# Kernel optimization log

Measured on AMD Instinct MI355X. Metric: run time of the kernel, lower is better.

Reference implementation:

```python
import jax, jax.numpy as jnp
import numpy as np

# dims: P planes, N planar nodes/plane, M nexus nodes, E edges/plane, C classes
P, N, M, E, C, FP, FN = 3, 100000, 30000, 200000, 5, 64, 32


def class_linear(x, W, b):
    # x: [..., C, in], W: [C, out, in], b: [C, out] -> [..., C, out]
    return jnp.einsum('...ci,coi->...co', x, W) + b


def setup_inputs() -> dict:
    key = jax.random.key(0)
    ks = jax.random.split(key, 12)
    def nrm(k, shape, scale=1.0):
        return jax.random.normal(k, shape, jnp.float32) * scale
    return {
        'x': nrm(ks[0], (P, N, C, FP)),
        'nexus': nrm(ks[1], (M, C, FN)),
        'edge_src': jax.random.randint(ks[2], (P, E), 0, N, jnp.int32),
        'edge_dst': jax.random.randint(ks[3], (P, E), 0, M, jnp.int32),
        'Wn1': nrm(ks[4], (C, FN, P * FP), (P * FP) ** -0.5),
        'bn1': jnp.zeros((C, FN), jnp.float32),
        'Wn2': nrm(ks[5], (C, FN, FN), FN ** -0.5),
        'bn2': jnp.zeros((C, FN), jnp.float32),
        'We': nrm(ks[6], (P, C, 1, FP + FN), (FP + FN) ** -0.5),
        'be': jnp.zeros((P, C, 1), jnp.float32),
        'Wd1': nrm(ks[7], (P, C, FP, FP + FN), (FP + FN) ** -0.5),
        'bd1': jnp.zeros((P, C, FP), jnp.float32),
        'Wd2': nrm(ks[8], (P, C, FP, FP), FP ** -0.5),
        'bd2': jnp.zeros((P, C, FP), jnp.float32),
    }


def reference(x, nexus, edge_src, edge_dst, Wn1, bn1, Wn2, bn2,
              We, be, Wd1, bd1, Wd2, bd2):
    # --- nexus_up: SimpleConv (sum-aggregate planar features at nexus nodes) ---
    def up_one(xp, src, dst):
        return jax.ops.segment_sum(xp[src], dst, num_segments=M)  # [M,C,FP]
    up = jax.vmap(up_one)(x, edge_src, edge_dst)                   # [P,M,C,FP]
    # torch.cat(n, dim=-1) over planes -> [M, C, P*FP]
    n_cat = jnp.transpose(up, (1, 2, 0, 3)).reshape(M, C, P * FP)

    # --- nexus_net: ClassLinear -> tanh -> ClassLinear -> tanh ---
    n = jnp.tanh(class_linear(n_cat, Wn1, bn1))
    n = jnp.tanh(class_linear(n, Wn2, bn2))                        # [M,C,FN]

    # --- nexus_down per plane (flow target_to_source, aggr mean at src) ---
    def down_one(xp, src, dst, We_p, be_p, W1, b1, W2, b2):
        x_i = xp[src]                                              # [E,C,FP]
        n_j = n[dst]                                               # [E,C,FN]
        feat = jax.lax.stop_gradient(jnp.concatenate([x_i, n_j], -1))
        # per-class scalar logit, softmax over class dim (dim=1)
        w = jax.nn.softmax(class_linear(feat, We_p, be_p), axis=1)  # [E,C,1]
        msg = w * n_j                                               # [E,C,FN]
        s = jax.ops.segment_sum(msg, src, num_segments=N)           # [N,C,FN]
        cnt = jax.ops.segment_sum(jnp.ones((E,), msg.dtype), src, num_segments=N)
        aggr = s / jnp.maximum(cnt, 1.0)[:, None, None]             # scatter-mean
        h = jnp.tanh(class_linear(jnp.concatenate([xp, aggr], -1), W1, b1))
        return jnp.tanh(class_linear(h, W2, b2))                    # [N,C,FP]

    out = jax.vmap(down_one)(x, edge_src, edge_dst, We, be, Wd1, bd1, Wd2, bd2)
    return out  # [P,N,C,FP] updated planar embeddings (x['u'],x['v'],x['y'])
```

## Files before the change

kernel.cpp:

```cpp
#include <hip/hip_runtime.h>
#include <hip/hip_fp16.h>

#define P_ 3
#define N_ 100000
#define M_ 30000
#define E_ 200000
#define C_ 5
#define FP_ 64
#define FN_ 32
#define PFP_ 192
#define FPFN_ 96
#define PE_ 600000
#define PN_ 300000
#define PM_ 90000
#define NT_ 64
#define TILES_ ((N_ + NT_ - 1) / NT_)
#define NTD_ 128
#define TILESD_ ((N_ + NTD_ - 1) / NTD_)
#define CFN_ 160
#define NW1_ 92160
#define NW2_ 61440
#define NWN1_ 30720
#define NB_S_ ((PN_ + 1023) / 1024)
#define NB_D_ ((PM_ + 1023) / 1024)
#define NB_CNT_ ((PE_ + 255) / 256)
#define NB_WC_ ((NW1_ + 255) / 256)
#define NB_PROJ_ (P_ * TILES_)
#define NB_FILL_ ((PE_ + 511) / 512)

typedef _Float16 f16x8 __attribute__((ext_vector_type(8)));
typedef float f32x4 __attribute__((ext_vector_type(4)));

__device__ __forceinline__ float fast_tanh(float v) {
  float t = __expf(2.0f * v);
  return 1.0f - __fdividef(2.0f, t + 1.0f);
}

__device__ __forceinline__ f16x8 ld8(const __half* p) {
  return *(const f16x8*)(const void*)p;
}

__global__ void k_countw(const int* __restrict__ esrc, const int* __restrict__ edst,
                         int* __restrict__ cnt_src, int* __restrict__ cnt_dst,
                         const float* __restrict__ Wd1, const float* __restrict__ Wd2,
                         const float* __restrict__ Wn1,
                         __half* __restrict__ w1h, __half* __restrict__ w2h,
                         __half* __restrict__ wn1h) {
  int b = blockIdx.x;
  if (b < NB_CNT_) {
    int i = b * 256 + threadIdx.x;
    if (i >= PE_) return;
    int p = i / E_;
    atomicAdd(&cnt_src[p * N_ + esrc[i]], 1);
    atomicAdd(&cnt_dst[p * M_ + edst[i]], 1);
  } else {
    int i = (b - NB_CNT_) * 256 + threadIdx.x;
    if (i < NW1_) w1h[i] = __float2half(Wd1[i]);
    if (i < NW2_) w2h[i] = __float2half(Wd2[i]);
    if (i < NWN1_) wn1h[i] = __float2half(Wn1[i]);
  }
}

__global__ void k_scan1c(const int* __restrict__ in_s, int* __restrict__ out_s,
                         int* __restrict__ aux_s,
                         const int* __restrict__ in_d, int* __restrict__ out_d,
                         int* __restrict__ aux_d) {
  __shared__ int lds[256];
  int b = blockIdx.x, t = threadIdx.x;
  const int* in;
  int* out;
  int* aux;
  int n;
  if (b < NB_S_) { in = in_s; out = out_s; aux = aux_s; n = PN_; }
  else           { b -= NB_S_; in = in_d; out = out_d; aux = aux_d; n = PM_; }
  int base = b * 1024 + t * 4;
  int v0 = (base + 0 < n) ? in[base + 0] : 0;
  int v1 = (base + 1 < n) ? in[base + 1] : 0;
  int v2 = (base + 2 < n) ? in[base + 2] : 0;
  int v3 = (base + 3 < n) ? in[base + 3] : 0;
  lds[t] = v0 + v1 + v2 + v3;
  __syncthreads();
  for (int off = 1; off < 256; off <<= 1) {
    int xv = (t >= off) ? lds[t - off] : 0;
    __syncthreads();
    lds[t] += xv;
    __syncthreads();
  }
  if (t == 255) aux[b] = lds[255];
  int run = (t == 0) ? 0 : lds[t - 1];
  if (base + 0 < n) out[base + 0] = run; run += v0;
  if (base + 1 < n) out[base + 1] = run; run += v1;
  if (base + 2 < n) out[base + 2] = run; run += v2;
  if (base + 3 < n) out[base + 3] = run;
}

__global__ void k_scan2c(int* __restrict__ aux_s, int* __restrict__ end_s,
                         int* __restrict__ aux_d, int* __restrict__ end_d) {
  __shared__ int lds[1024];
  int t = threadIdx.x;
  int* aux = (blockIdx.x == 0) ? aux_s : aux_d;
  int* offe = (blockIdx.x == 0) ? end_s : end_d;
  int nb = (blockIdx.x == 0) ? NB_S_ : NB_D_;
  lds[t] = (t < nb) ? aux[t] : 0;
  __syncthreads();
  for (int off = 1; off < 1024; off <<= 1) {
    int xv = (t >= off) ? lds[t - off] : 0;
    __syncthreads();
    lds[t] += xv;
    __syncthreads();
  }
  if (t < nb) aux[t] = (t == 0) ? 0 : lds[t - 1];
  if (t == 0) offe[0] = lds[nb - 1];
}

__global__ void k_scan3c(int* __restrict__ off_s, const int* __restrict__ aux_s,
                         int* __restrict__ cur_s,
                         int* __restrict__ off_d, const int* __restrict__ aux_d,
                         int* __restrict__ cur_d) {
  int i = blockIdx.x * 256 + threadIdx.x;
  if (i < PN_) {
    int v = off_s[i] + aux_s[i >> 10];
    off_s[i] = v;
    cur_s[i] = v;
  } else if (i < PN_ + PM_) {
    int j = i - PN_;
    int v = off_d[j] + aux_d[j >> 10];
    off_d[j] = v;
    cur_d[j] = v;
  }
}

__global__ __launch_bounds__(512) void k_projfill(
    const float* __restrict__ x, const __half* __restrict__ wn1h,
    const float* __restrict__ We,
    __half* __restrict__ y, float* __restrict__ xdot,
    __half* __restrict__ xh, int write_xh,
    const int* __restrict__ esrc, const int* __restrict__ edst,
    int* __restrict__ cur_src, int* __restrict__ cur_dst,
    int* __restrict__ list_src, int* __restrict__ list_src_e,
    int* __restrict__ list_dst, int* __restrict__ list_dst_e) {
  __shared__ __align__(16) __half xs[NT_ * 320];
  int bp = blockIdx.x;
  int t = threadIdx.x;

  if (bp >= NB_PROJ_) {
    int i = (bp - NB_PROJ_) * 512 + t;
    if (i < PE_) {
      int p = i / E_;
      int s = esrc[i], d = edst[i];
      int ps = atomicAdd(&cur_src[p * N_ + s], 1);
      list_src[ps] = d;
      list_src_e[ps] = i;
      int pd = atomicAdd(&cur_dst[p * M_ + d], 1);
      list_dst[pd] = s;
      list_dst_e[pd] = i;
    }
    return;
  }

  int p = bp / TILES_, tile = bp % TILES_;
  int base = tile * NT_;
  int rows = min(NT_, N_ - base);

  const float* xb = x + (size_t)(p * N_ + base) * 320;
  __half* xo = xh + (size_t)(p * N_ + base) * 320;
  for (int idx = t; idx < rows * 40; idx += 512) {
    int row = idx / 40, col = idx % 40;
    const float4* s4 = (const float4*)&xb[row * 320 + col * 8];
    float4 v0 = s4[0], v1 = s4[1];
    union { __half2 h[4]; float4 f; } u4;
    u4.h[0] = __floats2half2_rn(v0.x, v0.y);
    u4.h[1] = __floats2half2_rn(v0.z, v0.w);
    u4.h[2] = __floats2half2_rn(v1.x, v1.y);
    u4.h[3] = __floats2half2_rn(v1.z, v1.w);
    *(float4*)&xs[row * 320 + ((col * 8) ^ ((row & 7) << 3))] = u4.f;
    if (write_xh) *(float4*)&xo[row * 320 + col * 8] = u4.f;
  }
  __syncthreads();

  int w = t >> 6, l = t & 63;
  int l15 = l & 15, l4 = l >> 4;
  int q4 = w & 3, ct = w >> 2;
  int nA = q4 * 16 + l15;
  int swzA = (nA & 7) << 3;

  #pragma unroll
  for (int c = 0; c < C_; ++c) {
    f16x8 a0 = ld8(&xs[nA * 320 + ((c * 64 + 0  + l4 * 8) ^ swzA)]);
    f16x8 a1 = ld8(&xs[nA * 320 + ((c * 64 + 32 + l4 * 8) ^ swzA)]);
    const __half* wb = &wn1h[(size_t)(c * 32 + ct * 16 + l15) * PFP_ + p * 64];
    f16x8 b0 = ld8(&wb[0  + l4 * 8]);
    f16x8 b1 = ld8(&wb[32 + l4 * 8]);
    f32x4 acc = (f32x4){0.f, 0.f, 0.f, 0.f};
    acc = __builtin_amdgcn_mfma_f32_16x16x32_f16(a0, b0, acc, 0, 0, 0);
    acc = __builtin_amdgcn_mfma_f32_16x16x32_f16(a1, b1, acc, 0, 0, 0);
    #pragma unroll
    for (int r = 0; r < 4; ++r) {
      int node = q4 * 16 + l4 * 4 + r;
      if (node < rows)
        y[(size_t)(p * N_ + base + node) * CFN_ + c * 32 + ct * 16 + l15] =
            __float2half(acc[r]);
    }
  }

  for (int idx = t; idx < C_ * NT_; idx += 512) {
    int cx = idx >> 6, nodex = idx & 63;
    if (nodex < rows) {
      int swz = (nodex & 7) << 3;
      const float2* wer = (const float2*)&We[(p * C_ + cx) * FPFN_];
      float s = 0.f;
      #pragma unroll
      for (int i = 0; i < 32; ++i) {
        __half2 xv = *(const __half2*)&xs[nodex * 320 + ((cx * 64 + 2 * i) ^ swz)];
        float2 wv = wer[i];
        s += __low2float(xv) * wv.x + __high2float(xv) * wv.y;
      }
      xdot[(size_t)(p * N_ + base + nodex) * C_ + cx] = s;
    }
  }
}

__global__ __launch_bounds__(320) void k_nexus(
    const __half* __restrict__ y,
    const int* __restrict__ off_dst, const int* __restrict__ list_dst,
    const int* __restrict__ list_dst_e, const int* __restrict__ esrc,
    const float* __restrict__ bn1,
    const float* __restrict__ Wn2, const float* __restrict__ bn2,
    const float* __restrict__ We,
    const float* __restrict__ xdot, const float* __restrict__ be,
    __half* __restrict__ nout, __half* __restrict__ wbuf) {
  __shared__ float part[16][CFN_];
  __shared__ __align__(16) float h1S[CFN_];
  __shared__ __align__(16) float h2S[CFN_];
  __shared__ float ndS[P_ * C_];
  __shared__ float beS[P_ * C_];
  int m = blockIdx.x;
  int t = threadIdx.x;
  int g = t / 20, u4 = t % 20;

  float acc[8];
  #pragma unroll
  for (int i = 0; i < 8; ++i) acc[i] = 0.f;
  #pragma unroll
  for (int p = 0; p < P_; ++p) {
    int o0 = off_dst[p * M_ + m];
    int o1 = off_dst[p * M_ + m + 1];
    const __half* yp = y + (size_t)p * N_ * CFN_;
    for (int e = o0 + g; e < o1; e += 16) {
      int s0 = list_dst[e];
      float4 v = *(const float4*)&yp[(size_t)s0 * CFN_ + u4 * 8];
      union { float4 f; __half2 h[4]; } uu;
      uu.f = v;
      #pragma unroll
      for (int i = 0; i < 4; ++i) {
        acc[2 * i]     += __low2float(uu.h[i]);
        acc[2 * i + 1] += __high2float(uu.h[i]);
      }
    }
  }
  #pragma unroll
  for (int i = 0; i < 8; ++i) part[g][u4 * 8 + i] = acc[i];
  __syncthreads();
  if (t < CFN_) {
    float pre = bn1[t];
    #pragma unroll
    for (int gg = 0; gg < 16; ++gg) pre += part[gg][t];
    h1S[t] = fast_tanh(pre);
  }
  __syncthreads();
  if (t < CFN_) {
    int c = t >> 5;
    const float4* f4 = (const float4*)&h1S[c * FN_];
    const float4* w4 = (const float4*)&Wn2[(size_t)t * FN_];
    float a = bn2[t];
    #pragma unroll
    for (int i = 0; i < FN_ / 4; ++i) {
      float4 f = f4[i], wv = w4[i];
      a += f.x * wv.x + f.y * wv.y + f.z * wv.z + f.w * wv.w;
    }
    float nv = fast_tanh(a);
    h2S[t] = nv;
    nout[(size_t)m * CFN_ + t] = __float2half(nv);
  }
  __syncthreads();
  if (t < P_ * C_) {
    int p = t / C_, cc = t % C_;
    const float* wv = &We[(p * C_ + cc) * FPFN_ + FP_];
    float a = 0.f;
    #pragma unroll
    for (int j = 0; j < FN_; ++j) a += h2S[cc * FN_ + j] * wv[j];
    ndS[t] = a;
    beS[t] = be[t];
  }
  __syncthreads();
  #pragma unroll
  for (int p = 0; p < P_; ++p) {
    int o0 = off_dst[p * M_ + m];
    int o1 = off_dst[p * M_ + m + 1];
    for (int e = o0 + t; e < o1; e += 320) {
      int i = list_dst_e[e];
      int src = esrc[i];
      const float* xd = &xdot[(size_t)(p * N_ + src) * C_];
      float lg[C_];
      #pragma unroll
      for (int cc = 0; cc < C_; ++cc) lg[cc] = xd[cc] + ndS[p * C_ + cc] + beS[p * C_ + cc];
      float mx = fmaxf(fmaxf(fmaxf(lg[0], lg[1]), fmaxf(lg[2], lg[3])), lg[4]);
      float s = 0.f;
      #pragma unroll
      for (int cc = 0; cc < C_; ++cc) { lg[cc] = __expf(lg[cc] - mx); s += lg[cc]; }
      float inv = __fdividef(1.0f, s);
      __half* wp = &wbuf[(size_t)i * C_];
      #pragma unroll
      for (int cc = 0; cc < C_; ++cc) wp[cc] = __float2half(lg[cc] * inv);
    }
  }
}

template<int XH>
__global__ __launch_bounds__(256, 6) void k_dec(
    const float* __restrict__ x, const __half* __restrict__ xh,
    const __half* __restrict__ nout, const __half* __restrict__ wbuf,
    const int* __restrict__ off_src, const int* __restrict__ list_src,
    const int* __restrict__ list_src_e,
    const __half* __restrict__ w1h, const float* __restrict__ bd1,
    const __half* __restrict__ w2h, const float* __restrict__ bd2,
    float* __restrict__ out) {
  __shared__ __align__(16) __half featS[NTD_ * 104];

  int bp = blockIdx.x;
  int pc = bp / TILESD_;
  int tile = bp % TILESD_;
  int p = pc / C_, c = pc % C_;
  int base = tile * NTD_;
  int rows = min(NTD_, N_ - base);

  int t = threadIdx.x;
  int w = t >> 6, l = t & 63;
  int l15 = l & 15, l4 = l >> 4;

  if constexpr (XH) {
    for (int idx = t; idx < NTD_ * 8; idx += 256) {
      int node = idx >> 3, q = idx & 7;
      if (node < rows) {
        float4 v = *(const float4*)&xh[(size_t)(p * N_ + base + node) * 320 + c * 64 + q * 8];
        *(float4*)&featS[node * 104 + q * 8] = v;
      }
    }
  } else {
    for (int idx = t; idx < NTD_ * 16; idx += 256) {
      int node = idx >> 4, fq = idx & 15;
      if (node < rows) {
        float4 v = *(const float4*)&x[(size_t)(p * N_ + base + node) * 320 + c * 64 + fq * 4];
        __half2* dst = (__half2*)&featS[node * 104 + fq * 4];
        dst[0] = __floats2half2_rn(v.x, v.y);
        dst[1] = __floats2half2_rn(v.z, v.w);
      }
    }
  }
  {
    int nd = t >> 1, hf = t & 1;
    if (nd < rows) {
      int pn = p * N_ + base + nd;
      int o0 = off_src[pn], o1 = off_src[pn + 1];
      __half2 acc[8];
      #pragma unroll
      for (int i = 0; i < 8; ++i) acc[i] = __floats2half2_rn(0.f, 0.f);
      for (int e = o0; e < o1; e += 2) {
        int e1 = e + 1;
        bool has1 = (e1 < o1);
        int d0 = list_src[e];
        int i0 = list_src_e[e];
        int d1 = list_src[has1 ? e1 : e];
        int i1 = list_src_e[has1 ? e1 : e];
        __half wg0h = wbuf[(size_t)i0 * C_ + c];
        __half wg1h = wbuf[(size_t)i1 * C_ + c];
        const __half2* nr0 = (const __half2*)&nout[(size_t)d0 * CFN_ + c * FN_ + hf * 16];
        const __half2* nr1 = (const __half2*)&nout[(size_t)d1 * CFN_ + c * FN_ + hf * 16];
        __half2 v0[8], v1[8];
        #pragma unroll
        for (int i = 0; i < 8; ++i) v0[i] = nr0[i];
        #pragma unroll
        for (int i = 0; i < 8; ++i) v1[i] = nr1[i];
        __half2 wg0 = __half2half2(wg0h);
        #pragma unroll
        for (int i = 0; i < 8; ++i) acc[i] = __hfma2(wg0, v0[i], acc[i]);
        if (has1) {
          __half2 wg1 = __half2half2(wg1h);
          #pragma unroll
          for (int i = 0; i < 8; ++i) acc[i] = __hfma2(wg1, v1[i], acc[i]);
        }
      }
      float invd = __fdividef(1.0f, fmaxf((float)(o1 - o0), 1.0f));
      __half2 invd2 = __float2half2_rn(invd);
      __half2* dst2 = (__half2*)&featS[nd * 104 + 64 + hf * 16];
      #pragma unroll
      for (int i = 0; i < 8; ++i) dst2[i] = __hmul2(acc[i], invd2);
    }
  }
  __syncthreads();

  int rbase = w * 32;
  const __half* w1g = w1h + (size_t)(p * C_ + c) * 64 * 96;
  const __half* w2g = w2h + (size_t)(p * C_ + c) * 64 * 64;

  f32x4 acc[2][4];
  #pragma unroll
  for (int tt = 0; tt < 4; ++tt) {
    float bv = bd1[(p * C_ + c) * FP_ + tt * 16 + l15];
    #pragma unroll
    for (int rt = 0; rt < 2; ++rt) acc[rt][tt] = (f32x4){bv, bv, bv, bv};
  }
  #pragma unroll
  for (int s = 0; s < 3; ++s) {
    f16x8 a0 = ld8(&featS[(rbase + l15) * 104 + s * 32 + l4 * 8]);
    f16x8 a1 = ld8(&featS[(rbase + 16 + l15) * 104 + s * 32 + l4 * 8]);
    #pragma unroll
    for (int tt = 0; tt < 4; ++tt) {
      f16x8 b = ld8(&w1g[(tt * 16 + l15) * 96 + s * 32 + l4 * 8]);
      acc[0][tt] = __builtin_amdgcn_mfma_f32_16x16x32_f16(a0, b, acc[0][tt], 0, 0, 0);
      acc[1][tt] = __builtin_amdgcn_mfma_f32_16x16x32_f16(a1, b, acc[1][tt], 0, 0, 0);
    }
  }
  #pragma unroll
  for (int rt = 0; rt < 2; ++rt)
    #pragma unroll
    for (int tt = 0; tt < 4; ++tt) {
      #pragma unroll
      for (int r = 0; r < 4; ++r) {
        int nrow = rbase + rt * 16 + l4 * 4 + r;
        featS[nrow * 104 + tt * 16 + l15] = __float2half(fast_tanh(acc[rt][tt][r]));
      }
    }

  f32x4 acc2[2][4];
  #pragma unroll
  for (int tt = 0; tt < 4; ++tt) {
    float bv = bd2[(p * C_ + c) * FP_ + tt * 16 + l15];
    #pragma unroll
    for (int rt = 0; rt < 2; ++rt) acc2[rt][tt] = (f32x4){bv, bv, bv, bv};
  }
  #pragma unroll
  for (int s = 0; s < 2; ++s) {
    f16x8 a0 = ld8(&featS[(rbase + l15) * 104 + s * 32 + l4 * 8]);
    f16x8 a1 = ld8(&featS[(rbase + 16 + l15) * 104 + s * 32 + l4 * 8]);
    #pragma unroll
    for (int tt = 0; tt < 4; ++tt) {
      f16x8 b = ld8(&w2g[(tt * 16 + l15) * 64 + s * 32 + l4 * 8]);
      acc2[0][tt] = __builtin_amdgcn_mfma_f32_16x16x32_f16(a0, b, acc2[0][tt], 0, 0, 0);
      acc2[1][tt] = __builtin_amdgcn_mfma_f32_16x16x32_f16(a1, b, acc2[1][tt], 0, 0, 0);
    }
  }
  #pragma unroll
  for (int rt = 0; rt < 2; ++rt)
    #pragma unroll
    for (int tt = 0; tt < 4; ++tt) {
      #pragma unroll
      for (int r = 0; r < 4; ++r) {
        int nrow = rbase + rt * 16 + l4 * 4 + r;
        int node = base + nrow;
        if (node < N_) {
          out[(size_t)(p * N_ + node) * 320 + c * 64 + tt * 16 + l15] =
              fast_tanh(acc2[rt][tt][r]);
        }
      }
    }
}

#define WS_Y      0ll
#define WS_NOUT   24000000ll
#define WS_LISTSE 26400000ll
#define WS_WBUF   27000000ll
#define WS_XDOT   28800000ll
#define WS_OFFS   30750000ll
#define WS_OFFD   31050001ll
#define WS_CURS   31140002ll
#define WS_CURD   31440002ll
#define WS_LISTS  31530002ll
#define WS_LISTD  32130002ll
#define WS_AUX1   32730002ll
#define WS_AUX2   32730514ll
#define WS_W1H    32731026ll
#define WS_W2H    32777106ll
#define WS_LISTDE 32808000ll
#define WS_WN1H   33408000ll
#define WS_XH     33423360ll
#define WS_XH_END_BYTES ((WS_XH + 48000000ll) * 4ll)

extern "C" void kernel_launch(void* const* d_in, const int* in_sizes, int n_in,
                              void* d_out, int out_size, void* d_ws, size_t ws_size,
                              hipStream_t stream) {
  const float* x   = (const float*)d_in[0];
  const int* esrc  = (const int*)d_in[2];
  const int* edst  = (const int*)d_in[3];
  const float* Wn1 = (const float*)d_in[4];
  const float* bn1 = (const float*)d_in[5];
  const float* Wn2 = (const float*)d_in[6];
  const float* bn2 = (const float*)d_in[7];
  const float* We  = (const float*)d_in[8];
  const float* be  = (const float*)d_in[9];
  const float* Wd1 = (const float*)d_in[10];
  const float* bd1 = (const float*)d_in[11];
  const float* Wd2 = (const float*)d_in[12];
  const float* bd2 = (const float*)d_in[13];
  float* out = (float*)d_out;

  float* wsf = (float*)d_ws;
  int*   wsi = (int*)d_ws;
  __half* ybuf = (__half*)d_ws;
  __half* nout = (__half*)(wsi + WS_NOUT);
  __half* wbuf = (__half*)(wsi + WS_WBUF);
  float* xdot = wsf + WS_XDOT;
  int* off_src = wsi + WS_OFFS;
  int* off_dst = wsi + WS_OFFD;
  int* cur_src = wsi + WS_CURS;
  int* cur_dst = wsi + WS_CURD;
  int* list_src = wsi + WS_LISTS;
  int* list_src_e = wsi + WS_LISTSE;
  int* list_dst = wsi + WS_LISTD;
  int* list_dst_e = wsi + WS_LISTDE;
  int* aux1 = wsi + WS_AUX1;
  int* aux2 = wsi + WS_AUX2;
  __half* w1h = (__half*)(wsi + WS_W1H);
  __half* w2h = (__half*)(wsi + WS_W2H);
  __half* wn1h = (__half*)(wsi + WS_WN1H);
  __half* xh  = (__half*)(wsi + WS_XH);

  int use_xh = (ws_size >= (size_t)WS_XH_END_BYTES) ? 1 : 0;

  hipMemsetAsync(cur_src, 0, (PN_ + PM_) * sizeof(int), stream);
  k_countw<<<NB_CNT_ + NB_WC_, 256, 0, stream>>>(esrc, edst, cur_src, cur_dst,
                                                 Wd1, Wd2, Wn1, w1h, w2h, wn1h);
  k_scan1c<<<NB_S_ + NB_D_, 256, 0, stream>>>(cur_src, off_src, aux1,
                                              cur_dst, off_dst, aux2);
  k_scan2c<<<2, 1024, 0, stream>>>(aux1, off_src + PN_, aux2, off_dst + PM_);
  k_scan3c<<<(PN_ + PM_ + 255) / 256, 256, 0, stream>>>(off_src, aux1, cur_src,
                                                        off_dst, aux2, cur_dst);

  k_projfill<<<NB_PROJ_ + NB_FILL_, 512, 0, stream>>>(
      x, wn1h, We, ybuf, xdot, xh, use_xh,
      esrc, edst, cur_src, cur_dst,
      list_src, list_src_e, list_dst, list_dst_e);

  k_nexus<<<M_, 320, 0, stream>>>(ybuf, off_dst, list_dst, list_dst_e, esrc,
                                  bn1, Wn2, bn2, We, xdot, be, nout, wbuf);

  if (use_xh) {
    k_dec<1><<<P_ * C_ * TILESD_, 256, 0, stream>>>(x, xh, nout, wbuf,
                                                    off_src, list_src, list_src_e,
                                                    w1h, bd1, w2h, bd2, out);
  } else {
    k_dec<0><<<P_ * C_ * TILESD_, 256, 0, stream>>>(x, xh, nout, wbuf,
                                                    off_src, list_src, list_src_e,
                                                    w1h, bd1, w2h, bd2, out);
  }
}
```

Before: 718.5 us.

## Store softmax weights in src-CSR order and prefetch first edges in decoder

The fill step now records each edge's position in the source-sorted CSR list instead of storing the edge id there. The nexus kernel writes softmax weights at that CSR position, so the decoder reads weights contiguously by CSR index and no longer needs the list_src_e indirection. The decoder also loads offsets, the first two neighbor ids and their weights before staging the x tile, so those latencies overlap the tile load. This trades a scattered read of pos_src in k_nexus for fewer dependent gathers in the decoder.

```diff
diff --git a/kernel.cpp b/kernel.cpp
--- a/kernel.cpp
+++ b/kernel.cpp
@@ -137,7 +137,7 @@
     __half* __restrict__ xh, int write_xh,
     const int* __restrict__ esrc, const int* __restrict__ edst,
     int* __restrict__ cur_src, int* __restrict__ cur_dst,
-    int* __restrict__ list_src, int* __restrict__ list_src_e,
+    int* __restrict__ list_src, int* __restrict__ pos_src,
     int* __restrict__ list_dst, int* __restrict__ list_dst_e) {
   __shared__ __align__(16) __half xs[NT_ * 320];
   int bp = blockIdx.x;
@@ -150,7 +150,7 @@
       int s = esrc[i], d = edst[i];
       int ps = atomicAdd(&cur_src[p * N_ + s], 1);
       list_src[ps] = d;
-      list_src_e[ps] = i;
+      pos_src[i] = ps;
       int pd = atomicAdd(&cur_dst[p * M_ + d], 1);
       list_dst[pd] = s;
       list_dst_e[pd] = i;
@@ -224,6 +224,7 @@
     const __half* __restrict__ y,
     const int* __restrict__ off_dst, const int* __restrict__ list_dst,
     const int* __restrict__ list_dst_e, const int* __restrict__ esrc,
+    const int* __restrict__ pos_src,
     const float* __restrict__ bn1,
     const float* __restrict__ Wn2, const float* __restrict__ bn2,
     const float* __restrict__ We,
@@ -300,6 +301,7 @@
     for (int e = o0 + t; e < o1; e += 320) {
       int i = list_dst_e[e];
       int src = esrc[i];
+      int pos = pos_src[i];
       const float* xd = &xdot[(size_t)(p * N_ + src) * C_];
       float lg[C_];
       #pragma unroll
@@ -309,7 +311,7 @@
       #pragma unroll
       for (int cc = 0; cc < C_; ++cc) { lg[cc] = __expf(lg[cc] - mx); s += lg[cc]; }
       float inv = __fdividef(1.0f, s);
-      __half* wp = &wbuf[(size_t)i * C_];
+      __half* wp = &wbuf[(size_t)pos * C_];
       #pragma unroll
       for (int cc = 0; cc < C_; ++cc) wp[cc] = __float2half(lg[cc] * inv);
     }
@@ -321,7 +323,6 @@
     const float* __restrict__ x, const __half* __restrict__ xh,
     const __half* __restrict__ nout, const __half* __restrict__ wbuf,
     const int* __restrict__ off_src, const int* __restrict__ list_src,
-    const int* __restrict__ list_src_e,
     const __half* __restrict__ w1h, const float* __restrict__ bd1,
     const __half* __restrict__ w2h, const float* __restrict__ bd2,
     float* __restrict__ out) {
@@ -337,6 +338,22 @@
   int t = threadIdx.x;
   int w = t >> 6, l = t & 63;
   int l15 = l & 15, l4 = l >> 4;
+
+  int nd = t >> 1, hf = t & 1;
+  int o0 = 0, o1 = 0, d0 = 0, d1 = 0;
+  __half wg0h = __float2half(0.f), wg1h = __float2half(0.f);
+  bool nact = (nd < rows);
+  if (nact) {
+    int pn = p * N_ + base + nd;
+    o0 = off_src[pn];
+    o1 = off_src[pn + 1];
+    int e1 = o0 + 1;
+    bool has1 = (e1 < o1);
+    d0 = (o0 < o1) ? list_src[o0] : 0;
+    d1 = has1 ? list_src[e1] : d0;
+    if (o0 < o1) wg0h = wbuf[(size_t)o0 * C_ + c];
+    if (has1)    wg1h = wbuf[(size_t)e1 * C_ + c];
+  }
 
   if constexpr (XH) {
     for (int idx = t; idx < NTD_ * 8; idx += 256) {
@@ -357,45 +374,41 @@
       }
     }
   }
-  {
-    int nd = t >> 1, hf = t & 1;
-    if (nd < rows) {
-      int pn = p * N_ + base + nd;
-      int o0 = off_src[pn], o1 = off_src[pn + 1];
-      __half2 acc[8];
-      #pragma unroll
-      for (int i = 0; i < 8; ++i) acc[i] = __floats2half2_rn(0.f, 0.f);
-      for (int e = o0; e < o1; e += 2) {
-        int e1 = e + 1;
-        bool has1 = (e1 < o1);
-        int d0 = list_src[e];
-        int i0 = list_src_e[e];
-        int d1 = list_src[has1 ? e1 : e];
-        int i1 = list_src_e[has1 ? e1 : e];
-        __half wg0h = wbuf[(size_t)i0 * C_ + c];
-        __half wg1h = wbuf[(size_t)i1 * C_ + c];
-        const __half2* nr0 = (const __half2*)&nout[(size_t)d0 * CFN_ + c * FN_ + hf * 16];
-        const __half2* nr1 = (const __half2*)&nout[(size_t)d1 * CFN_ + c * FN_ + hf * 16];
-        __half2 v0[8], v1[8];
+
+  if (nact) {
+    __half2 acc[8];
+    #pragma unroll
+    for (int i = 0; i < 8; ++i) acc[i] = __floats2half2_rn(0.f, 0.f);
+    if (o0 < o1) {
+      const __half2* nr0 = (const __half2*)&nout[(size_t)d0 * CFN_ + c * FN_ + hf * 16];
+      const __half2* nr1 = (const __half2*)&nout[(size_t)d1 * CFN_ + c * FN_ + hf * 16];
+      bool has1 = (o0 + 1 < o1);
+      __half2 v0[8], v1[8];
+      #pragma unroll
+      for (int i = 0; i < 8; ++i) v0[i] = nr0[i];
+      #pragma unroll
+      for (int i = 0; i < 8; ++i) v1[i] = nr1[i];
+      __half2 wg0 = __half2half2(wg0h);
+      #pragma unroll
+      for (int i = 0; i < 8; ++i) acc[i] = __hfma2(wg0, v0[i], acc[i]);
+      if (has1) {
+        __half2 wg1 = __half2half2(wg1h);
         #pragma unroll
-        for (int i = 0; i < 8; ++i) v0[i] = nr0[i];
+        for (int i = 0; i < 8; ++i) acc[i] = __hfma2(wg1, v1[i], acc[i]);
+      }
+      for (int e = o0 + 2; e < o1; ++e) {
+        int dd = list_src[e];
+        __half2 wg = __half2half2(wbuf[(size_t)e * C_ + c]);
+        const __half2* nr = (const __half2*)&nout[(size_t)dd * CFN_ + c * FN_ + hf * 16];
         #pragma unroll
-        for (int i = 0; i < 8; ++i) v1[i] = nr1[i];
-        __half2 wg0 = __half2half2(wg0h);
-        #pragma unroll
-        for (int i = 0; i < 8; ++i) acc[i] = __hfma2(wg0, v0[i], acc[i]);
-        if (has1) {
-          __half2 wg1 = __half2half2(wg1h);
-          #pragma unroll
-          for (int i = 0; i < 8; ++i) acc[i] = __hfma2(wg1, v1[i], acc[i]);
-        }
-      }
-      float invd = __fdividef(1.0f, fmaxf((float)(o1 - o0), 1.0f));
-      __half2 invd2 = __float2half2_rn(invd);
-      __half2* dst2 = (__half2*)&featS[nd * 104 + 64 + hf * 16];
-      #pragma unroll
-      for (int i = 0; i < 8; ++i) dst2[i] = __hmul2(acc[i], invd2);
-    }
+        for (int i = 0; i < 8; ++i) acc[i] = __hfma2(wg, nr[i], acc[i]);
+      }
+    }
+    float invd = __fdividef(1.0f, fmaxf((float)(o1 - o0), 1.0f));
+    __half2 invd2 = __float2half2_rn(invd);
+    __half2* dst2 = (__half2*)&featS[nd * 104 + 64 + hf * 16];
+    #pragma unroll
+    for (int i = 0; i < 8; ++i) dst2[i] = __hmul2(acc[i], invd2);
   }
   __syncthreads();
 
@@ -468,7 +481,7 @@
 
 #define WS_Y      0ll
 #define WS_NOUT   24000000ll
-#define WS_LISTSE 26400000ll
+#define WS_POSS   26400000ll
 #define WS_WBUF   27000000ll
 #define WS_XDOT   28800000ll
 #define WS_OFFS   30750000ll
@@ -515,7 +528,7 @@
   int* cur_src = wsi + WS_CURS;
   int* cur_dst = wsi + WS_CURD;
   int* list_src = wsi + WS_LISTS;
-  int* list_src_e = wsi + WS_LISTSE;
+  int* pos_src = wsi + WS_POSS;
   int* list_dst = wsi + WS_LISTD;
   int* list_dst_e = wsi + WS_LISTDE;
   int* aux1 = wsi + WS_AUX1;
@@ -539,18 +552,19 @@
   k_projfill<<<NB_PROJ_ + NB_FILL_, 512, 0, stream>>>(
       x, wn1h, We, ybuf, xdot, xh, use_xh,
       esrc, edst, cur_src, cur_dst,
-      list_src, list_src_e, list_dst, list_dst_e);
+      list_src, pos_src, list_dst, list_dst_e);
 
   k_nexus<<<M_, 320, 0, stream>>>(ybuf, off_dst, list_dst, list_dst_e, esrc,
-                                  bn1, Wn2, bn2, We, xdot, be, nout, wbuf);
+                                  pos_src, bn1, Wn2, bn2, We, xdot, be,
+                                  nout, wbuf);
 
   if (use_xh) {
     k_dec<1><<<P_ * C_ * TILESD_, 256, 0, stream>>>(x, xh, nout, wbuf,
-                                                    off_src, list_src, list_src_e,
+                                                    off_src, list_src,
                                                     w1h, bd1, w2h, bd2, out);
   } else {
     k_dec<0><<<P_ * C_ * TILESD_, 256, 0, stream>>>(x, xh, nout, wbuf,
-                                                    off_src, list_src, list_src_e,
+                                                    off_src, list_src,
                                                     w1h, bd1, w2h, bd2, out);
   }
 }
```

Measured after the change: 733.5 us. 2.1% more time.
